# Kernel optimization log

Hardware: AMD Instinct MI355X
Metric: run time of the kernel (lower is better)

The kernel has to match this reference:

```python
import jax, jax.numpy as jnp
import numpy as np

GH, GW, B, H, OUT = 9, 9, 1024, 256, 1


def setup_inputs() -> dict:
    key = jax.random.key(0)
    ks = jax.random.split(key, 16)
    N = GH * GW
    s3 = 1.0 / np.sqrt(3 * H)
    sH = 1.0 / np.sqrt(H)
    return {
        "x": jax.random.normal(ks[0], (B, GH, GW), jnp.float32),
        "h_ext": jax.random.normal(ks[1], (B, H), jnp.float32),
        "c_ext": jax.random.normal(ks[2], (B, H), jnp.float32),
        "grid_h": jax.random.normal(ks[3], (GH, GW, B, H), jnp.float32),
        "grid_c": jax.random.normal(ks[4], (GH, GW, B, H), jnp.float32),
        "W_hp": jax.random.normal(ks[5], (N, H, 3 * H), jnp.float32) * s3,
        "b_hp": jax.random.normal(ks[6], (N, H), jnp.float32) * s3,
        "W_cp": jax.random.normal(ks[7], (N, H, 3 * H), jnp.float32) * s3,
        "b_cp": jax.random.normal(ks[8], (N, H), jnp.float32) * s3,
        "W_ih": jax.random.normal(ks[9], (N, 4 * H, 1), jnp.float32) * sH,
        "W_hh": jax.random.normal(ks[10], (N, 4 * H, H), jnp.float32) * sH,
        "b_ih": jax.random.normal(ks[11], (N, 4 * H), jnp.float32) * sH,
        "b_hh": jax.random.normal(ks[12], (N, 4 * H), jnp.float32) * sH,
        "W_out": jax.random.normal(ks[13], (OUT, H), jnp.float32) * sH,
        "b_out": jnp.zeros((OUT,), jnp.float32),
    }


def _lstm_cell(x_cell, h0, c0, W_ih_k, W_hh_k, b_ih_k, b_hh_k):
    # x_cell: [B,1], h0/c0: [B,H]; torch LSTMCell math
    gates = x_cell @ W_ih_k.T + b_ih_k + h0 @ W_hh_k.T + b_hh_k  # [B,4H]
    i, f, g, o = jnp.split(gates, 4, axis=1)
    i, f, o = jax.nn.sigmoid(i), jax.nn.sigmoid(f), jax.nn.sigmoid(o)
    g = jnp.tanh(g)
    c = f * c0 + i * g
    h = o * jnp.tanh(c)
    return h, c


def reference(x, h_ext, c_ext, grid_h, grid_c,
              W_hp, b_hp, W_cp, b_cp,
              W_ih, W_hh, b_ih, b_hh, W_out, b_out):
    zeros = jnp.zeros((B, H), x.dtype)
    # new states, updated in raster order; left/up neighbors read NEW states
    new_h = [[None] * GW for _ in range(GH)]
    new_c = [[None] * GW for _ in range(GH)]
    for i in range(GH):
        for j in range(GW):
            k = i * GW + j
            h_prev, c_prev = grid_h[i, j], grid_c[i, j]
            if i == 0 and j == 0:
                h_left, c_left = h_ext, c_ext
            elif j > 0:
                h_left, c_left = new_h[i][j - 1], new_c[i][j - 1]
            else:
                h_left, c_left = zeros, zeros
            if i > 0:
                h_up, c_up = new_h[i - 1][j], new_c[i - 1][j]
            else:
                h_up, c_up = zeros, zeros
            comb_h = jnp.concatenate([h_left, h_up, h_prev], axis=1)  # [B,3H]
            comb_c = jnp.concatenate([c_left, c_up, c_prev], axis=1)
            ph = comb_h @ W_hp[k].T + b_hp[k]
            pc = comb_c @ W_cp[k].T + b_cp[k]
            x_cell = x[:, i, j][:, None]  # [B,1]
            h_new, c_new = _lstm_cell(x_cell, ph, pc, W_ih[k], W_hh[k], b_ih[k], b_hh[k])
            new_h[i][j], new_c[i][j] = h_new, c_new
    final_h, final_c = new_h[-1][-1], new_c[-1][-1]
    # fc_out with fc_layers_out=[0]: Linear + ReLU, then sigmoid
    out = jax.nn.sigmoid(jax.nn.relu(final_h @ W_out.T + b_out))
    gh = jnp.stack([jnp.stack(r, 0) for r in new_h], 0)
    gc = jnp.stack([jnp.stack(r, 0) for r in new_c], 0)
    return out, final_h, final_c, gh, gc
```

## Files before the change

kernel.cpp:

```cpp
#include <hip/hip_runtime.h>
#include <math.h>

#define BATCH 1024
#define HID 256
#define W3 768
#define SLOT (BATCH * HID)

typedef __bf16 bf16_t;
typedef __bf16 bf16x8 __attribute__((ext_vector_type(8)));
typedef __bf16 bf16x4 __attribute__((ext_vector_type(4)));
typedef float f32x4 __attribute__((ext_vector_type(4)));

__device__ inline bf16x8 cvt8(const float4 a, const float4 b) {
    bf16x8 r;
    r[0] = (bf16_t)a.x; r[1] = (bf16_t)a.y; r[2] = (bf16_t)a.z; r[3] = (bf16_t)a.w;
    r[4] = (bf16_t)b.x; r[5] = (bf16_t)b.y; r[6] = (bf16_t)b.z; r[7] = (bf16_t)b.w;
    return r;
}
__device__ inline bf16x4 cvt4(const float4 a) {
    bf16x4 r;
    r[0] = (bf16_t)a.x; r[1] = (bf16_t)a.y; r[2] = (bf16_t)a.z; r[3] = (bf16_t)a.w;
    return r;
}

__global__ __launch_bounds__(256) void compose_kernel(
        const float* __restrict__ Whh, const float* __restrict__ Whp,
        bf16_t* __restrict__ CC) {
    __shared__ bf16_t As[128][40];
    __shared__ bf16_t Bs[128][40];
    const int k = blockIdx.z;
    const int t = threadIdx.x;
    const int lane = t & 63, wid = t >> 6;
    const int wm = wid & 1, wn = wid >> 1;
    const int ln = lane & 15, lh = lane >> 4;
    const int m0 = blockIdx.x * 128;
    const int by = blockIdx.y;
    const int sr = t >> 1, sq = (t & 1) * 16;
    const int g_r = sr >> 5, du_r = sr & 31;
    const float* arow = Whh + (size_t)k * 4 * HID * HID
                        + (size_t)(g_r * HID + by * 32 + du_r) * HID + sq;
    const float* wbase = Whp + (size_t)k * HID * W3;
    const int uu = t >> 3, mm0 = (t & 7) * 16;
    f32x4 acc[4][4] = {};
    for (int kb = 0; kb < 8; ++kb) {
        const float4 a0 = *(const float4*)(arow + kb * 32);
        const float4 a1 = *(const float4*)(arow + kb * 32 + 4);
        const float4 a2 = *(const float4*)(arow + kb * 32 + 8);
        const float4 a3 = *(const float4*)(arow + kb * 32 + 12);
        const float* bsrc = wbase + (size_t)(kb * 32 + uu) * W3 + m0 + mm0;
        const float4 v0 = *(const float4*)(bsrc);
        const float4 v1 = *(const float4*)(bsrc + 4);
        const float4 v2 = *(const float4*)(bsrc + 8);
        const float4 v3 = *(const float4*)(bsrc + 12);
        const bf16x8 av0 = cvt8(a0, a1), av1 = cvt8(a2, a3);
        const bf16x4 bq[4] = { cvt4(v0), cvt4(v1), cvt4(v2), cvt4(v3) };
        __syncthreads();
        *(bf16x8*)&As[sr][sq] = av0;
        *(bf16x8*)&As[sr][sq + 8] = av1;
        #pragma unroll
        for (int q = 0; q < 4; ++q)
            #pragma unroll
            for (int e = 0; e < 4; ++e)
                Bs[mm0 + q * 4 + e][uu] = bq[q][e];
        __syncthreads();
        bf16x8 af[4], bfv[4];
        #pragma unroll
        for (int mf = 0; mf < 4; ++mf)
            af[mf] = *(const bf16x8*)&As[wm * 64 + mf * 16 + ln][lh * 8];
        #pragma unroll
        for (int nf = 0; nf < 4; ++nf)
            bfv[nf] = *(const bf16x8*)&Bs[wn * 64 + nf * 16 + ln][lh * 8];
        #pragma unroll
        for (int mf = 0; mf < 4; ++mf)
            #pragma unroll
            for (int nf = 0; nf < 4; ++nf)
                acc[mf][nf] = __builtin_amdgcn_mfma_f32_16x16x32_bf16(
                    af[mf], bfv[nf], acc[mf][nf], 0, 0, 0);
    }
    bf16_t* outp = CC + (size_t)k * 1024 * W3;
    #pragma unroll
    for (int nf = 0; nf < 4; ++nf) {
        const int m = m0 + wn * 64 + nf * 16 + ln;
        #pragma unroll
        for (int mf = 0; mf < 4; ++mf)
            #pragma unroll
            for (int r = 0; r < 4; ++r) {
                const int c = by * 128 + wm * 64 + mf * 16 + lh * 4 + r;
                outp[(size_t)c * W3 + m] = (bf16_t)acc[mf][nf][r];
            }
    }
}

__global__ __launch_bounds__(256) void gvec_kernel(
        const float* __restrict__ Whh, const float* __restrict__ bhp,
        const float* __restrict__ bih, const float* __restrict__ bhh,
        float* __restrict__ gvec) {
    const int k = blockIdx.x, t = threadIdx.x;
    __shared__ float bsm[HID];
    bsm[t] = bhp[(size_t)k * HID + t];
    __syncthreads();
    #pragma unroll
    for (int g = 0; g < 4; ++g) {
        const int n4 = g * HID + t;
        const float* wr = Whh + (size_t)k * 4 * HID * HID + (size_t)n4 * HID;
        float s = 0.f;
        for (int u = 0; u < HID; u += 4) {
            const float4 w = *(const float4*)(wr + u);
            s += w.x * bsm[u] + w.y * bsm[u + 1] + w.z * bsm[u + 2] + w.w * bsm[u + 3];
        }
        gvec[(size_t)k * 1024 + n4] = s + bih[(size_t)k * 1024 + n4]
                                        + bhh[(size_t)k * 1024 + n4];
    }
}

struct StageDesc {
    const float* hs0; const float* cs0;
    const float* hs1; const float* cs1;
    const float* hs2; const float* cs2;
    const bf16_t* cc;
    const float* wcp;
    const float* gvec;
    const float* wih;
    const float* bcp;
    const float* xk;
    float* gh; float* gc;
};
struct StageArgs { StageDesc d[9]; };

__global__ __launch_bounds__(256) void stage_kernel(StageArgs args) {
    const StageDesc sd = args.d[blockIdx.z];
    __shared__ bf16_t A1[128][40];
    __shared__ bf16_t A2[128][40];
    __shared__ bf16_t B1[128][40];
    __shared__ bf16_t B2[32][40];
    const int t = threadIdx.x;
    const int lane = t & 63, wid = t >> 6;
    const int wm = wid & 1, wn = wid >> 1;
    const int ln = lane & 15, lh = lane >> 4;
    const int b0 = blockIdx.x * 128;
    const int by = blockIdx.y, u0 = by * 32;
    const int sr = t >> 1, sq = (t & 1) * 16;
    const int du2 = t >> 3, kk4 = (t & 7) * 4;

    const float* hs[3] = { sd.hs0, sd.hs1, sd.hs2 };
    const float* cs[3] = { sd.cs0, sd.cs1, sd.cs2 };

    f32x4 accg[4][4] = {};
    f32x4 accp[4] = {};

    for (int s = 0; s < 3; ++s) {
        if (!hs[s]) continue;
        const int ko = s * 256;
        const float* ha = hs[s] + (size_t)(b0 + sr) * HID + sq;
        const float* ca = cs[s] + (size_t)(b0 + sr) * HID + sq;
        const bf16_t* b1r = sd.cc + (size_t)(by * 128 + sr) * W3 + ko + sq;
        const float* b2r = sd.wcp + (size_t)(u0 + du2) * W3 + ko + kk4;
        for (int kb = 0; kb < 8; ++kb) {
            const float4 h0 = *(const float4*)(ha + kb * 32);
            const float4 h1 = *(const float4*)(ha + kb * 32 + 4);
            const float4 h2 = *(const float4*)(ha + kb * 32 + 8);
            const float4 h3 = *(const float4*)(ha + kb * 32 + 12);
            const float4 c0 = *(const float4*)(ca + kb * 32);
            const float4 c1 = *(const float4*)(ca + kb * 32 + 4);
            const float4 c2 = *(const float4*)(ca + kb * 32 + 8);
            const float4 c3 = *(const float4*)(ca + kb * 32 + 12);
            const bf16x8 w0 = *(const bf16x8*)(b1r + kb * 32);
            const bf16x8 w1 = *(const bf16x8*)(b1r + kb * 32 + 8);
            const float4 p0 = *(const float4*)(b2r + kb * 32);
            const bf16x8 hv0 = cvt8(h0, h1), hv1 = cvt8(h2, h3);
            const bf16x8 cv0 = cvt8(c0, c1), cv1 = cvt8(c2, c3);
            const bf16x4 pv = cvt4(p0);
            __syncthreads();
            *(bf16x8*)&A1[sr][sq] = hv0;
            *(bf16x8*)&A1[sr][sq + 8] = hv1;
            *(bf16x8*)&A2[sr][sq] = cv0;
            *(bf16x8*)&A2[sr][sq + 8] = cv1;
            *(bf16x8*)&B1[sr][sq] = w0;
            *(bf16x8*)&B1[sr][sq + 8] = w1;
            *(bf16x4*)&B2[du2][kk4] = pv;
            __syncthreads();
            bf16x8 af1[4], af2[4], bf1[4], bf2;
            #pragma unroll
            for (int mf = 0; mf < 4; ++mf) {
                af1[mf] = *(const bf16x8*)&A1[wm * 64 + mf * 16 + ln][lh * 8];
                af2[mf] = *(const bf16x8*)&A2[wm * 64 + mf * 16 + ln][lh * 8];
            }
            #pragma unroll
            for (int g = 0; g < 4; ++g)
                bf1[g] = *(const bf16x8*)&B1[g * 32 + wn * 16 + ln][lh * 8];
            bf2 = *(const bf16x8*)&B2[wn * 16 + ln][lh * 8];
            #pragma unroll
            for (int mf = 0; mf < 4; ++mf) {
                #pragma unroll
                for (int g = 0; g < 4; ++g)
                    accg[mf][g] = __builtin_amdgcn_mfma_f32_16x16x32_bf16(
                        af1[mf], bf1[g], accg[mf][g], 0, 0, 0);
                accp[mf] = __builtin_amdgcn_mfma_f32_16x16x32_bf16(
                    af2[mf], bf2, accp[mf], 0, 0, 0);
            }
        }
    }

    const int u = u0 + wn * 16 + ln;
    float wih[4], gv[4];
    #pragma unroll
    for (int g = 0; g < 4; ++g) {
        const int n4 = g * HID + u;
        wih[g] = sd.wih[n4];
        gv[g] = sd.gvec[n4];
    }
    const float bc = sd.bcp[u];
    #pragma unroll
    for (int mf = 0; mf < 4; ++mf)
        #pragma unroll
        for (int r = 0; r < 4; ++r) {
            const int b = b0 + wm * 64 + mf * 16 + lh * 4 + r;
            const float xv = sd.xk[(size_t)b * 81];
            const float gi = accg[mf][0][r] + gv[0] + xv * wih[0];
            const float gf = accg[mf][1][r] + gv[1] + xv * wih[1];
            const float gg = accg[mf][2][r] + gv[2] + xv * wih[2];
            const float go = accg[mf][3][r] + gv[3] + xv * wih[3];
            const float pc = accp[mf][r] + bc;
            const float i_ = 1.f / (1.f + expf(-gi));
            const float f_ = 1.f / (1.f + expf(-gf));
            const float o_ = 1.f / (1.f + expf(-go));
            const float g_ = tanhf(gg);
            const float cn = f_ * pc + i_ * g_;
            const float hn = o_ * tanhf(cn);
            sd.gh[(size_t)b * HID + u] = hn;
            sd.gc[(size_t)b * HID + u] = cn;
        }
}

__global__ __launch_bounds__(256) void final_kernel(
        const float* __restrict__ gh88, const float* __restrict__ gc88,
        const float* __restrict__ Wout, const float* __restrict__ bout,
        float* __restrict__ out, float* __restrict__ fh, float* __restrict__ fc) {
    const int tid = blockIdx.x * blockDim.x + threadIdx.x;
    const int nth = gridDim.x * blockDim.x;
    for (int idx = tid; idx < BATCH * HID; idx += nth) {
        fh[idx] = gh88[idx];
        fc[idx] = gc88[idx];
    }
    if (tid < BATCH) {
        float s = bout[0];
        for (int k = 0; k < HID; ++k) s += gh88[(size_t)tid * HID + k] * Wout[k];
        s = fmaxf(s, 0.f);
        out[tid] = 1.f / (1.f + expf(-s));
    }
}

template<bool ATOMIC>
__device__ __forceinline__ void proj_core(
        const float* __restrict__ src, const float* __restrict__ W, int koff,
        const float* __restrict__ bias, float* __restrict__ out,
        bf16_t (*Asm)[40], bf16_t (*Bsm)[40]) {
    const int t = threadIdx.x;
    const int lane = t & 63, wid = t >> 6;
    const int wm = wid & 1, wn = wid >> 1;
    const int ln = lane & 15, lh = lane >> 4;
    const int b0 = blockIdx.x * 128, n0 = blockIdx.y * 128;
    const int sr = t >> 1, sq = (t & 1) * 16;
    const float* arow = src + (size_t)(b0 + sr) * HID + sq;
    const float* wrow = W + (size_t)(n0 + sr) * W3 + koff + sq;
    f32x4 acc[4][4] = {};
    for (int kb = 0; kb < 8; ++kb) {
        const float4 a0 = *(const float4*)(arow + kb * 32);
        const float4 a1 = *(const float4*)(arow + kb * 32 + 4);
        const float4 a2 = *(const float4*)(arow + kb * 32 + 8);
        const float4 a3 = *(const float4*)(arow + kb * 32 + 12);
        const float4 w0 = *(const float4*)(wrow + kb * 32);
        const float4 w1 = *(const float4*)(wrow + kb * 32 + 4);
        const float4 w2 = *(const float4*)(wrow + kb * 32 + 8);
        const float4 w3 = *(const float4*)(wrow + kb * 32 + 12);
        const bf16x8 av0 = cvt8(a0, a1), av1 = cvt8(a2, a3);
        const bf16x8 bv0 = cvt8(w0, w1), bv1 = cvt8(w2, w3);
        __syncthreads();
        *(bf16x8*)&Asm[sr][sq] = av0;
        *(bf16x8*)&Asm[sr][sq + 8] = av1;
        *(bf16x8*)&Bsm[sr][sq] = bv0;
        *(bf16x8*)&Bsm[sr][sq + 8] = bv1;
        __syncthreads();
        bf16x8 af[4], bfv[4];
        #pragma unroll
        for (int mf = 0; mf < 4; ++mf)
            af[mf] = *(const bf16x8*)&Asm[wm * 64 + mf * 16 + ln][lh * 8];
        #pragma unroll
        for (int nf = 0; nf < 4; ++nf)
            bfv[nf] = *(const bf16x8*)&Bsm[wn * 64 + nf * 16 + ln][lh * 8];
        #pragma unroll
        for (int mf = 0; mf < 4; ++mf)
            #pragma unroll
            for (int nf = 0; nf < 4; ++nf)
                acc[mf][nf] = __builtin_amdgcn_mfma_f32_16x16x32_bf16(
                    af[mf], bfv[nf], acc[mf][nf], 0, 0, 0);
    }
    #pragma unroll
    for (int nf = 0; nf < 4; ++nf) {
        const int n = n0 + wn * 64 + nf * 16 + ln;
        const float bn = ATOMIC ? 0.f : bias[n];
        #pragma unroll
        for (int mf = 0; mf < 4; ++mf)
            #pragma unroll
            for (int r = 0; r < 4; ++r) {
                const int b = b0 + wm * 64 + mf * 16 + lh * 4 + r;
                if (ATOMIC)
                    unsafeAtomicAdd(out + (size_t)b * HID + n, acc[mf][nf][r]);
                else
                    out[(size_t)b * HID + n] = acc[mf][nf][r] + bn;
            }
    }
}

struct SegDesc { const float* src; const float* W; const float* bias; float* out; int koff; };
struct SegArgs { SegDesc d[36]; };

__global__ __launch_bounds__(256) void projseg_kernel(SegArgs a) {
    __shared__ bf16_t As[128][40];
    __shared__ bf16_t Bs[128][40];
    const SegDesc d = a.d[blockIdx.z];
    if (d.bias) proj_core<false>(d.src, d.W, d.koff, d.bias, d.out, As, Bs);
    else        proj_core<true>(d.src, d.W, d.koff, nullptr, d.out, As, Bs);
}

struct CellDesc {
    const float* ph; const float* pc;
    const float* Whh; const float* Wih; const float* bih; const float* bhh;
    const float* xcol;
    float* gh; float* gc;
};
struct CellBatchArgs { CellDesc d[9]; };

__global__ __launch_bounds__(256) void cell_kernel(CellBatchArgs args) {
    const CellDesc cd = args.d[blockIdx.z];
    __shared__ bf16_t Psm[128][40];
    __shared__ bf16_t Wsm[128][40];
    const int t = threadIdx.x;
    const int lane = t & 63, wid = t >> 6;
    const int wm = wid & 1, wn = wid >> 1;
    const int ln = lane & 15, lh = lane >> 4;
    const int b0 = blockIdx.x * 128;
    const int u0 = blockIdx.y * 32;
    const int sr = t >> 1, sq = (t & 1) * 16;
    const float* prow = cd.ph + (size_t)(b0 + sr) * HID + sq;
    const int cg = sr >> 5, cdu = sr & 31;
    const float* wrow = cd.Whh + (size_t)(cg * HID + u0 + cdu) * HID + sq;
    f32x4 acc[4][4] = {};
    for (int kb = 0; kb < 8; ++kb) {
        const float4 p0 = *(const float4*)(prow + kb * 32);
        const float4 p1 = *(const float4*)(prow + kb * 32 + 4);
        const float4 p2 = *(const float4*)(prow + kb * 32 + 8);
        const float4 p3 = *(const float4*)(prow + kb * 32 + 12);
        const float4 w0 = *(const float4*)(wrow + kb * 32);
        const float4 w1 = *(const float4*)(wrow + kb * 32 + 4);
        const float4 w2 = *(const float4*)(wrow + kb * 32 + 8);
        const float4 w3 = *(const float4*)(wrow + kb * 32 + 12);
        const bf16x8 pv0 = cvt8(p0, p1), pv1 = cvt8(p2, p3);
        const bf16x8 wv0 = cvt8(w0, w1), wv1 = cvt8(w2, w3);
        __syncthreads();
        *(bf16x8*)&Psm[sr][sq] = pv0;
        *(bf16x8*)&Psm[sr][sq + 8] = pv1;
        *(bf16x8*)&Wsm[sr][sq] = wv0;
        *(bf16x8*)&Wsm[sr][sq + 8] = wv1;
        __syncthreads();
        bf16x8 af[4], bfr[4];
        #pragma unroll
        for (int mf = 0; mf < 4; ++mf)
            af[mf] = *(const bf16x8*)&Psm[wm * 64 + mf * 16 + ln][lh * 8];
        #pragma unroll
        for (int g = 0; g < 4; ++g)
            bfr[g] = *(const bf16x8*)&Wsm[g * 32 + wn * 16 + ln][lh * 8];
        #pragma unroll
        for (int mf = 0; mf < 4; ++mf)
            #pragma unroll
            for (int g = 0; g < 4; ++g)
                acc[mf][g] = __builtin_amdgcn_mfma_f32_16x16x32_bf16(
                    af[mf], bfr[g], acc[mf][g], 0, 0, 0);
    }
    const int u = u0 + wn * 16 + ln;
    float wih[4], bsum[4];
    #pragma unroll
    for (int g = 0; g < 4; ++g) {
        const int n = g * HID + u;
        wih[g] = cd.Wih[n];
        bsum[g] = cd.bih[n] + cd.bhh[n];
    }
    #pragma unroll
    for (int mf = 0; mf < 4; ++mf)
        #pragma unroll
        for (int r = 0; r < 4; ++r) {
            const int b = b0 + wm * 64 + mf * 16 + lh * 4 + r;
            const float xv = cd.xcol[(size_t)b * 81];
            const float gi = acc[mf][0][r] + xv * wih[0] + bsum[0];
            const float gf = acc[mf][1][r] + xv * wih[1] + bsum[1];
            const float gg = acc[mf][2][r] + xv * wih[2] + bsum[2];
            const float go = acc[mf][3][r] + xv * wih[3] + bsum[3];
            const float i_ = 1.f / (1.f + expf(-gi));
            const float f_ = 1.f / (1.f + expf(-gf));
            const float o_ = 1.f / (1.f + expf(-go));
            const float g_ = tanhf(gg);
            const float c0 = cd.pc[(size_t)b * HID + u];
            const float cn = f_ * c0 + i_ * g_;
            const float hn = o_ * tanhf(cn);
            cd.gh[(size_t)b * HID + u] = hn;
            cd.gc[(size_t)b * HID + u] = cn;
        }
}

extern "C" void kernel_launch(void* const* d_in, const int* in_sizes, int n_in,
                              void* d_out, int out_size, void* d_ws, size_t ws_size,
                              hipStream_t stream) {
    const float* x      = (const float*)d_in[0];
    const float* h_ext  = (const float*)d_in[1];
    const float* c_ext  = (const float*)d_in[2];
    const float* grid_h = (const float*)d_in[3];
    const float* grid_c = (const float*)d_in[4];
    const float* W_hp   = (const float*)d_in[5];
    const float* b_hp   = (const float*)d_in[6];
    const float* W_cp   = (const float*)d_in[7];
    const float* b_cp   = (const float*)d_in[8];
    const float* W_ih   = (const float*)d_in[9];
    const float* W_hh   = (const float*)d_in[10];
    const float* b_ih   = (const float*)d_in[11];
    const float* b_hh   = (const float*)d_in[12];
    const float* W_out  = (const float*)d_in[13];
    const float* b_out  = (const float*)d_in[14];

    float* out = (float*)d_out;
    float* fh  = out + BATCH * 1;
    float* fc  = fh + SLOT;
    float* gh  = fc + SLOT;
    float* gc  = gh + (size_t)81 * SLOT;

    const size_t cc_bytes = (size_t)81 * 1024 * W3 * 2;
    const size_t gv_bytes = (size_t)81 * 1024 * 4;

    if (ws_size >= cc_bytes + gv_bytes) {
        bf16_t* CC = (bf16_t*)d_ws;
        float* gvec = (float*)((char*)d_ws + cc_bytes);

        compose_kernel<<<dim3(6, 8, 81), 256, 0, stream>>>(W_hh, W_hp, CC);
        gvec_kernel<<<dim3(81), 256, 0, stream>>>(W_hh, b_hp, b_ih, b_hh, gvec);

        for (int d = 0; d <= 16; ++d) {
            const int i_lo = d > 8 ? d - 8 : 0;
            const int i_hi = d < 8 ? d : 8;
            const int nc = i_hi - i_lo + 1;
            StageArgs sa{};
            for (int s = 0; s < nc; ++s) {
                const int i = i_lo + s, j = d - i;
                const int k = i * 9 + j;
                const float *hl = nullptr, *cl = nullptr, *hu = nullptr, *cu = nullptr;
                if (i == 0 && j == 0)      { hl = h_ext; cl = c_ext; }
                else if (j > 0)            { hl = gh + (size_t)(k - 1) * SLOT;
                                             cl = gc + (size_t)(k - 1) * SLOT; }
                if (i > 0)                 { hu = gh + (size_t)(k - 9) * SLOT;
                                             cu = gc + (size_t)(k - 9) * SLOT; }
                sa.d[s] = { hl, cl, hu, cu,
                            grid_h + (size_t)k * SLOT, grid_c + (size_t)k * SLOT,
                            CC + (size_t)k * 1024 * W3,
                            W_cp + (size_t)k * HID * W3,
                            gvec + (size_t)k * 1024,
                            W_ih + (size_t)k * 1024,
                            b_cp + (size_t)k * HID,
                            x + k,
                            gh + (size_t)k * SLOT,
                            gc + (size_t)k * SLOT };
            }
            stage_kernel<<<dim3(8, 8, nc), 256, 0, stream>>>(sa);
        }
    } else {
        float* ws = (float*)d_ws;
        for (int d = 0; d <= 16; ++d) {
            const int i_lo = d > 8 ? d - 8 : 0;
            const int i_hi = d < 8 ? d : 8;
            const int nc = i_hi - i_lo + 1;
            SegArgs base{}, inc{};
            CellBatchArgs ca{};
            int nb = 0, ni = 0;
            for (int s = 0; s < nc; ++s) {
                const int i = i_lo + s, j = d - i;
                const int k = i * 9 + j;
                float* oh = ws + (size_t)(2 * s) * SLOT;
                float* oc = oh + SLOT;
                const float* Wh = W_hp + (size_t)k * HID * W3;
                const float* Wc = W_cp + (size_t)k * HID * W3;
                base.d[nb++] = { grid_h + (size_t)k * SLOT, Wh, b_hp + (size_t)k * HID, oh, 512 };
                base.d[nb++] = { grid_c + (size_t)k * SLOT, Wc, b_cp + (size_t)k * HID, oc, 512 };
                if (i == 0 && j == 0) {
                    inc.d[ni++] = { h_ext, Wh, nullptr, oh, 0 };
                    inc.d[ni++] = { c_ext, Wc, nullptr, oc, 0 };
                } else if (j > 0) {
                    inc.d[ni++] = { gh + (size_t)(k - 1) * SLOT, Wh, nullptr, oh, 0 };
                    inc.d[ni++] = { gc + (size_t)(k - 1) * SLOT, Wc, nullptr, oc, 0 };
                }
                if (i > 0) {
                    inc.d[ni++] = { gh + (size_t)(k - 9) * SLOT, Wh, nullptr, oh, 256 };
                    inc.d[ni++] = { gc + (size_t)(k - 9) * SLOT, Wc, nullptr, oc, 256 };
                }
                ca.d[s] = { oh, oc,
                            W_hh + (size_t)k * 4 * HID * HID,
                            W_ih + (size_t)k * 4 * HID,
                            b_ih + (size_t)k * 4 * HID,
                            b_hh + (size_t)k * 4 * HID,
                            x + i * 9 + j,
                            gh + (size_t)k * SLOT,
                            gc + (size_t)k * SLOT };
            }
            projseg_kernel<<<dim3(8, 2, nb), 256, 0, stream>>>(base);
            projseg_kernel<<<dim3(8, 2, ni), 256, 0, stream>>>(inc);
            cell_kernel<<<dim3(8, 8, nc), 256, 0, stream>>>(ca);
        }
    }
    final_kernel<<<dim3(64), 256, 0, stream>>>(
        gh + (size_t)80 * SLOT, gc + (size_t)80 * SLOT,
        W_out, b_out, out, fh, fc);
}
```

Before: 1.229 ms.

## Precompute grid_prev gate contributions in one batched kernel, keep states in bf16

```diff
diff --git a/kernel.cpp b/kernel.cpp
--- a/kernel.cpp
+++ b/kernel.cpp
@@ -21,6 +21,48 @@
     bf16x4 r;
     r[0] = (bf16_t)a.x; r[1] = (bf16_t)a.y; r[2] = (bf16_t)a.z; r[3] = (bf16_t)a.w;
     return r;
+}
+
+__global__ __launch_bounds__(256) void prep_conv(
+        const float* __restrict__ wcp, bf16_t* __restrict__ wcpb,
+        const float* __restrict__ he, const float* __restrict__ ce,
+        bf16_t* __restrict__ heb, bf16_t* __restrict__ ceb) {
+    const size_t n1 = (size_t)81 * HID * W3;
+    const size_t n2 = (size_t)SLOT;
+    const size_t total4 = (n1 + 2 * n2) / 4;
+    size_t tid = (size_t)blockIdx.x * 256 + threadIdx.x;
+    const size_t nth = (size_t)gridDim.x * 256;
+    for (size_t i4 = tid; i4 < total4; i4 += nth) {
+        const size_t i = i4 * 4;
+        const float* s; bf16_t* dst; size_t off;
+        if (i < n1)            { s = wcp; dst = wcpb; off = i; }
+        else if (i < n1 + n2)  { s = he;  dst = heb;  off = i - n1; }
+        else                   { s = ce;  dst = ceb;  off = i - n1 - n2; }
+        const float4 v = *(const float4*)(s + off);
+        *(bf16x4*)(dst + off) = cvt4(v);
+    }
+}
+
+__global__ __launch_bounds__(256) void gvec_kernel(
+        const float* __restrict__ Whh, const float* __restrict__ bhp,
+        const float* __restrict__ bih, const float* __restrict__ bhh,
+        float* __restrict__ gvec) {
+    const int k = blockIdx.x, t = threadIdx.x;
+    __shared__ float bsm[HID];
+    bsm[t] = bhp[(size_t)k * HID + t];
+    __syncthreads();
+    #pragma unroll
+    for (int g = 0; g < 4; ++g) {
+        const int n4 = g * HID + t;
+        const float* wr = Whh + (size_t)k * 4 * HID * HID + (size_t)n4 * HID;
+        float s = 0.f;
+        for (int u = 0; u < HID; u += 4) {
+            const float4 w = *(const float4*)(wr + u);
+            s += w.x * bsm[u] + w.y * bsm[u + 1] + w.z * bsm[u + 2] + w.w * bsm[u + 3];
+        }
+        gvec[(size_t)k * 1024 + n4] = s + bih[(size_t)k * 1024 + n4]
+                                        + bhh[(size_t)k * 1024 + n4];
+    }
 }
 
 __global__ __launch_bounds__(256) void compose_kernel(
@@ -91,44 +133,13 @@
     }
 }
 
-__global__ __launch_bounds__(256) void gvec_kernel(
-        const float* __restrict__ Whh, const float* __restrict__ bhp,
-        const float* __restrict__ bih, const float* __restrict__ bhh,
-        float* __restrict__ gvec) {
-    const int k = blockIdx.x, t = threadIdx.x;
-    __shared__ float bsm[HID];
-    bsm[t] = bhp[(size_t)k * HID + t];
-    __syncthreads();
-    #pragma unroll
-    for (int g = 0; g < 4; ++g) {
-        const int n4 = g * HID + t;
-        const float* wr = Whh + (size_t)k * 4 * HID * HID + (size_t)n4 * HID;
-        float s = 0.f;
-        for (int u = 0; u < HID; u += 4) {
-            const float4 w = *(const float4*)(wr + u);
-            s += w.x * bsm[u] + w.y * bsm[u + 1] + w.z * bsm[u + 2] + w.w * bsm[u + 3];
-        }
-        gvec[(size_t)k * 1024 + n4] = s + bih[(size_t)k * 1024 + n4]
-                                        + bhh[(size_t)k * 1024 + n4];
-    }
-}
-
-struct StageDesc {
-    const float* hs0; const float* cs0;
-    const float* hs1; const float* cs1;
-    const float* hs2; const float* cs2;
-    const bf16_t* cc;
-    const float* wcp;
-    const float* gvec;
-    const float* wih;
-    const float* bcp;
-    const float* xk;
-    float* gh; float* gc;
-};
-struct StageArgs { StageDesc d[9]; };
-
-__global__ __launch_bounds__(256) void stage_kernel(StageArgs args) {
-    const StageDesc sd = args.d[blockIdx.z];
+__global__ __launch_bounds__(256) void prevgates_kernel(
+        const float* __restrict__ gridh, const float* __restrict__ gridc,
+        const bf16_t* __restrict__ CC, const bf16_t* __restrict__ Wcpb,
+        const float* __restrict__ gvec, const float* __restrict__ Wih,
+        const float* __restrict__ bcp, const float* __restrict__ x,
+        bf16_t* __restrict__ gp, bf16_t* __restrict__ pp) {
+    const int k = blockIdx.z;
     __shared__ bf16_t A1[128][40];
     __shared__ bf16_t A2[128][40];
     __shared__ bf16_t B1[128][40];
@@ -142,42 +153,132 @@
     const int sr = t >> 1, sq = (t & 1) * 16;
     const int du2 = t >> 3, kk4 = (t & 7) * 4;
 
-    const float* hs[3] = { sd.hs0, sd.hs1, sd.hs2 };
-    const float* cs[3] = { sd.cs0, sd.cs1, sd.cs2 };
+    const float* ha = gridh + (size_t)k * SLOT + (size_t)(b0 + sr) * HID + sq;
+    const float* ca = gridc + (size_t)k * SLOT + (size_t)(b0 + sr) * HID + sq;
+    const bf16_t* b1r = CC + (size_t)k * 1024 * W3 + (size_t)(by * 128 + sr) * W3 + 512 + sq;
+    const bf16_t* b2r = Wcpb + (size_t)k * HID * W3 + (size_t)(u0 + du2) * W3 + 512 + kk4;
 
     f32x4 accg[4][4] = {};
     f32x4 accp[4] = {};
-
-    for (int s = 0; s < 3; ++s) {
+    for (int kb = 0; kb < 8; ++kb) {
+        const float4 h0 = *(const float4*)(ha + kb * 32);
+        const float4 h1 = *(const float4*)(ha + kb * 32 + 4);
+        const float4 h2 = *(const float4*)(ha + kb * 32 + 8);
+        const float4 h3 = *(const float4*)(ha + kb * 32 + 12);
+        const float4 c0 = *(const float4*)(ca + kb * 32);
+        const float4 c1 = *(const float4*)(ca + kb * 32 + 4);
+        const float4 c2 = *(const float4*)(ca + kb * 32 + 8);
+        const float4 c3 = *(const float4*)(ca + kb * 32 + 12);
+        const bf16x8 w0 = *(const bf16x8*)(b1r + kb * 32);
+        const bf16x8 w1 = *(const bf16x8*)(b1r + kb * 32 + 8);
+        const bf16x4 p0 = *(const bf16x4*)(b2r + kb * 32);
+        const bf16x8 hv0 = cvt8(h0, h1), hv1 = cvt8(h2, h3);
+        const bf16x8 cv0 = cvt8(c0, c1), cv1 = cvt8(c2, c3);
+        __syncthreads();
+        *(bf16x8*)&A1[sr][sq] = hv0;  *(bf16x8*)&A1[sr][sq + 8] = hv1;
+        *(bf16x8*)&A2[sr][sq] = cv0;  *(bf16x8*)&A2[sr][sq + 8] = cv1;
+        *(bf16x8*)&B1[sr][sq] = w0;   *(bf16x8*)&B1[sr][sq + 8] = w1;
+        *(bf16x4*)&B2[du2][kk4] = p0;
+        __syncthreads();
+        bf16x8 af1[4], af2[4], bf1[4], bf2;
+        #pragma unroll
+        for (int mf = 0; mf < 4; ++mf) {
+            af1[mf] = *(const bf16x8*)&A1[wm * 64 + mf * 16 + ln][lh * 8];
+            af2[mf] = *(const bf16x8*)&A2[wm * 64 + mf * 16 + ln][lh * 8];
+        }
+        #pragma unroll
+        for (int g = 0; g < 4; ++g)
+            bf1[g] = *(const bf16x8*)&B1[g * 32 + wn * 16 + ln][lh * 8];
+        bf2 = *(const bf16x8*)&B2[wn * 16 + ln][lh * 8];
+        #pragma unroll
+        for (int mf = 0; mf < 4; ++mf) {
+            #pragma unroll
+            for (int g = 0; g < 4; ++g)
+                accg[mf][g] = __builtin_amdgcn_mfma_f32_16x16x32_bf16(
+                    af1[mf], bf1[g], accg[mf][g], 0, 0, 0);
+            accp[mf] = __builtin_amdgcn_mfma_f32_16x16x32_bf16(
+                af2[mf], bf2, accp[mf], 0, 0, 0);
+        }
+    }
+
+    const int u = u0 + wn * 16 + ln;
+    float wv[4], gv[4];
+    #pragma unroll
+    for (int g = 0; g < 4; ++g) {
+        const int n4 = g * HID + u;
+        wv[g] = Wih[(size_t)k * 1024 + n4];
+        gv[g] = gvec[(size_t)k * 1024 + n4];
+    }
+    const float bc = bcp[(size_t)k * HID + u];
+    bf16_t* gpk = gp + (size_t)k * BATCH * 1024;
+    bf16_t* ppk = pp + (size_t)k * SLOT;
+    #pragma unroll
+    for (int mf = 0; mf < 4; ++mf)
+        #pragma unroll
+        for (int r = 0; r < 4; ++r) {
+            const int b = b0 + wm * 64 + mf * 16 + lh * 4 + r;
+            const float xv = x[(size_t)b * 81 + k];
+            #pragma unroll
+            for (int g = 0; g < 4; ++g)
+                gpk[(size_t)b * 1024 + by * 128 + g * 32 + wn * 16 + ln] =
+                    (bf16_t)(accg[mf][g][r] + gv[g] + xv * wv[g]);
+            ppk[(size_t)b * HID + u] = (bf16_t)(accp[mf][r] + bc);
+        }
+}
+
+struct Stage2Desc {
+    const bf16_t* hs0; const bf16_t* cs0;
+    const bf16_t* hs1; const bf16_t* cs1;
+    const bf16_t* cc;
+    const bf16_t* wcpb;
+    const bf16_t* gp;
+    const bf16_t* pp;
+    float* gh; float* gc;
+    bf16_t* ghb; bf16_t* gcb;
+};
+struct Stage2Args { Stage2Desc d[9]; };
+
+__global__ __launch_bounds__(256) void stage2_kernel(Stage2Args args) {
+    const Stage2Desc sd = args.d[blockIdx.z];
+    __shared__ bf16_t A1[128][40];
+    __shared__ bf16_t A2[128][40];
+    __shared__ bf16_t B1[128][40];
+    __shared__ bf16_t B2[32][40];
+    const int t = threadIdx.x;
+    const int lane = t & 63, wid = t >> 6;
+    const int wm = wid & 1, wn = wid >> 1;
+    const int ln = lane & 15, lh = lane >> 4;
+    const int b0 = blockIdx.x * 128;
+    const int by = blockIdx.y, u0 = by * 32;
+    const int sr = t >> 1, sq = (t & 1) * 16;
+    const int du2 = t >> 3, kk4 = (t & 7) * 4;
+
+    const bf16_t* hs[2] = { sd.hs0, sd.hs1 };
+    const bf16_t* cs[2] = { sd.cs0, sd.cs1 };
+
+    f32x4 accg[4][4] = {};
+    f32x4 accp[4] = {};
+
+    for (int s = 0; s < 2; ++s) {
         if (!hs[s]) continue;
         const int ko = s * 256;
-        const float* ha = hs[s] + (size_t)(b0 + sr) * HID + sq;
-        const float* ca = cs[s] + (size_t)(b0 + sr) * HID + sq;
+        const bf16_t* ha = hs[s] + (size_t)(b0 + sr) * HID + sq;
+        const bf16_t* ca = cs[s] + (size_t)(b0 + sr) * HID + sq;
         const bf16_t* b1r = sd.cc + (size_t)(by * 128 + sr) * W3 + ko + sq;
-        const float* b2r = sd.wcp + (size_t)(u0 + du2) * W3 + ko + kk4;
+        const bf16_t* b2r = sd.wcpb + (size_t)(u0 + du2) * W3 + ko + kk4;
         for (int kb = 0; kb < 8; ++kb) {
-            const float4 h0 = *(const float4*)(ha + kb * 32);
-            const float4 h1 = *(const float4*)(ha + kb * 32 + 4);
-            const float4 h2 = *(const float4*)(ha + kb * 32 + 8);
-            const float4 h3 = *(const float4*)(ha + kb * 32 + 12);
-            const float4 c0 = *(const float4*)(ca + kb * 32);
-            const float4 c1 = *(const float4*)(ca + kb * 32 + 4);
-            const float4 c2 = *(const float4*)(ca + kb * 32 + 8);
-            const float4 c3 = *(const float4*)(ca + kb * 32 + 12);
+            const bf16x8 h0 = *(const bf16x8*)(ha + kb * 32);
+            const bf16x8 h1 = *(const bf16x8*)(ha + kb * 32 + 8);
+            const bf16x8 c0 = *(const bf16x8*)(ca + kb * 32);
+            const bf16x8 c1 = *(const bf16x8*)(ca + kb * 32 + 8);
             const bf16x8 w0 = *(const bf16x8*)(b1r + kb * 32);
             const bf16x8 w1 = *(const bf16x8*)(b1r + kb * 32 + 8);
-            const float4 p0 = *(const float4*)(b2r + kb * 32);
-            const bf16x8 hv0 = cvt8(h0, h1), hv1 = cvt8(h2, h3);
-            const bf16x8 cv0 = cvt8(c0, c1), cv1 = cvt8(c2, c3);
-            const bf16x4 pv = cvt4(p0);
+            const bf16x4 p0 = *(const bf16x4*)(b2r + kb * 32);
             __syncthreads();
-            *(bf16x8*)&A1[sr][sq] = hv0;
-            *(bf16x8*)&A1[sr][sq + 8] = hv1;
-            *(bf16x8*)&A2[sr][sq] = cv0;
-            *(bf16x8*)&A2[sr][sq + 8] = cv1;
-            *(bf16x8*)&B1[sr][sq] = w0;
-            *(bf16x8*)&B1[sr][sq + 8] = w1;
-            *(bf16x4*)&B2[du2][kk4] = pv;
+            *(bf16x8*)&A1[sr][sq] = h0;  *(bf16x8*)&A1[sr][sq + 8] = h1;
+            *(bf16x8*)&A2[sr][sq] = c0;  *(bf16x8*)&A2[sr][sq + 8] = c1;
+            *(bf16x8*)&B1[sr][sq] = w0;  *(bf16x8*)&B1[sr][sq + 8] = w1;
+            *(bf16x4*)&B2[du2][kk4] = p0;
             __syncthreads();
             bf16x8 af1[4], af2[4], bf1[4], bf2;
             #pragma unroll
@@ -202,25 +303,17 @@
     }
 
     const int u = u0 + wn * 16 + ln;
-    float wih[4], gv[4];
-    #pragma unroll
-    for (int g = 0; g < 4; ++g) {
-        const int n4 = g * HID + u;
-        wih[g] = sd.wih[n4];
-        gv[g] = sd.gvec[n4];
-    }
-    const float bc = sd.bcp[u];
     #pragma unroll
     for (int mf = 0; mf < 4; ++mf)
         #pragma unroll
         for (int r = 0; r < 4; ++r) {
             const int b = b0 + wm * 64 + mf * 16 + lh * 4 + r;
-            const float xv = sd.xk[(size_t)b * 81];
-            const float gi = accg[mf][0][r] + gv[0] + xv * wih[0];
-            const float gf = accg[mf][1][r] + gv[1] + xv * wih[1];
-            const float gg = accg[mf][2][r] + gv[2] + xv * wih[2];
-            const float go = accg[mf][3][r] + gv[3] + xv * wih[3];
-            const float pc = accp[mf][r] + bc;
+            const bf16_t* gpr = sd.gp + (size_t)b * 1024 + by * 128 + wn * 16 + ln;
+            const float gi = accg[mf][0][r] + (float)gpr[0];
+            const float gf = accg[mf][1][r] + (float)gpr[32];
+            const float gg = accg[mf][2][r] + (float)gpr[64];
+            const float go = accg[mf][3][r] + (float)gpr[96];
+            const float pc = accp[mf][r] + (float)sd.pp[(size_t)b * HID + u];
             const float i_ = 1.f / (1.f + expf(-gi));
             const float f_ = 1.f / (1.f + expf(-gf));
             const float o_ = 1.f / (1.f + expf(-go));
@@ -229,6 +322,8 @@
             const float hn = o_ * tanhf(cn);
             sd.gh[(size_t)b * HID + u] = hn;
             sd.gc[(size_t)b * HID + u] = cn;
+            sd.ghb[(size_t)b * HID + u] = (bf16_t)hn;
+            sd.gcb[(size_t)b * HID + u] = (bf16_t)cn;
         }
 }
 
@@ -432,42 +527,56 @@
     float* gh  = fc + SLOT;
     float* gc  = gh + (size_t)81 * SLOT;
 
-    const size_t cc_bytes = (size_t)81 * 1024 * W3 * 2;
-    const size_t gv_bytes = (size_t)81 * 1024 * 4;
-
-    if (ws_size >= cc_bytes + gv_bytes) {
-        bf16_t* CC = (bf16_t*)d_ws;
-        float* gvec = (float*)((char*)d_ws + cc_bytes);
-
+    const size_t cc_b  = (size_t)81 * 1024 * W3 * 2;
+    const size_t wcp_b = (size_t)81 * HID * W3 * 2;
+    const size_t gp_b  = (size_t)81 * BATCH * 1024 * 2;
+    const size_t pp_b  = (size_t)81 * SLOT * 2;
+    const size_t st_b  = (size_t)81 * SLOT * 2;
+    const size_t ext_b = (size_t)SLOT * 2;
+    const size_t gv_b  = (size_t)81 * 1024 * 4;
+    const size_t need = cc_b + wcp_b + gp_b + pp_b + 2 * st_b + 2 * ext_b + gv_b;
+
+    if (ws_size >= need) {
+        char* p = (char*)d_ws;
+        bf16_t* CC   = (bf16_t*)p; p += cc_b;
+        bf16_t* Wcpb = (bf16_t*)p; p += wcp_b;
+        bf16_t* GP   = (bf16_t*)p; p += gp_b;
+        bf16_t* PP   = (bf16_t*)p; p += pp_b;
+        bf16_t* GHB  = (bf16_t*)p; p += st_b;
+        bf16_t* GCB  = (bf16_t*)p; p += st_b;
+        bf16_t* HEB  = (bf16_t*)p; p += ext_b;
+        bf16_t* CEB  = (bf16_t*)p; p += ext_b;
+        float*  gvec = (float*)p;
+
+        prep_conv<<<dim3(2048), 256, 0, stream>>>(W_cp, Wcpb, h_ext, c_ext, HEB, CEB);
+        gvec_kernel<<<dim3(81), 256, 0, stream>>>(W_hh, b_hp, b_ih, b_hh, gvec);
         compose_kernel<<<dim3(6, 8, 81), 256, 0, stream>>>(W_hh, W_hp, CC);
-        gvec_kernel<<<dim3(81), 256, 0, stream>>>(W_hh, b_hp, b_ih, b_hh, gvec);
+        prevgates_kernel<<<dim3(8, 8, 81), 256, 0, stream>>>(
+            grid_h, grid_c, CC, Wcpb, gvec, W_ih, b_cp, x, GP, PP);
 
         for (int d = 0; d <= 16; ++d) {
             const int i_lo = d > 8 ? d - 8 : 0;
             const int i_hi = d < 8 ? d : 8;
             const int nc = i_hi - i_lo + 1;
-            StageArgs sa{};
+            Stage2Args sa{};
             for (int s = 0; s < nc; ++s) {
                 const int i = i_lo + s, j = d - i;
                 const int k = i * 9 + j;
-                const float *hl = nullptr, *cl = nullptr, *hu = nullptr, *cu = nullptr;
-                if (i == 0 && j == 0)      { hl = h_ext; cl = c_ext; }
-                else if (j > 0)            { hl = gh + (size_t)(k - 1) * SLOT;
-                                             cl = gc + (size_t)(k - 1) * SLOT; }
-                if (i > 0)                 { hu = gh + (size_t)(k - 9) * SLOT;
-                                             cu = gc + (size_t)(k - 9) * SLOT; }
+                const bf16_t *hl = nullptr, *cl = nullptr, *hu = nullptr, *cu = nullptr;
+                if (i == 0 && j == 0)      { hl = HEB; cl = CEB; }
+                else if (j > 0)            { hl = GHB + (size_t)(k - 1) * SLOT;
+                                             cl = GCB + (size_t)(k - 1) * SLOT; }
+                if (i > 0)                 { hu = GHB + (size_t)(k - 9) * SLOT;
+                                             cu = GCB + (size_t)(k - 9) * SLOT; }
                 sa.d[s] = { hl, cl, hu, cu,
-                            grid_h + (size_t)k * SLOT, grid_c + (size_t)k * SLOT,
                             CC + (size_t)k * 1024 * W3,
-                            W_cp + (size_t)k * HID * W3,
-                            gvec + (size_t)k * 1024,
-                            W_ih + (size_t)k * 1024,
-                            b_cp + (size_t)k * HID,
-                            x + k,
-                            gh + (size_t)k * SLOT,
-                            gc + (size_t)k * SLOT };
+                            Wcpb + (size_t)k * HID * W3,
+                            GP + (size_t)k * BATCH * 1024,
+                            PP + (size_t)k * SLOT,
+                            gh + (size_t)k * SLOT, gc + (size_t)k * SLOT,
+                            GHB + (size_t)k * SLOT, GCB + (size_t)k * SLOT };
             }
-            stage_kernel<<<dim3(8, 8, nc), 256, 0, stream>>>(sa);
+            stage2_kernel<<<dim3(8, 8, nc), 256, 0, stream>>>(sa);
         }
     } else {
         float* ws = (float*)d_ws;
```

New measurement: 1.124 ms. 1.09x faster.
